# Optimization experiments

Measured on AMD Instinct MI355X. Metric: run time of the kernel, lower is better.

The kernel has to match this reference:

```python
import jax, jax.numpy as jnp
import numpy as np

B, N, NFEAT, NHID, NOUT, H = 16, 1024, 128, 256, 256, 4
DH = NOUT // H  # 64 per head
EPS = 1e-5
ALPHA = 0.2  # LeakyReLU negative slope


def setup_inputs() -> dict:
    key = jax.random.key(0)
    ks = jax.random.split(key, 8)
    stdv = 1.0 / np.sqrt(NHID)
    return {
        "x": jax.random.normal(ks[0], (B, N, NFEAT), dtype=jnp.float32),
        "adj": jax.random.uniform(ks[1], (N, N), dtype=jnp.float32) / N,
        "gc_w": jax.random.uniform(ks[2], (NFEAT, NHID), minval=-stdv, maxval=stdv, dtype=jnp.float32),
        "gc_b": jax.random.uniform(ks[3], (NHID,), minval=-stdv, maxval=stdv, dtype=jnp.float32),
        "bn1_gamma": jnp.ones((NHID,), jnp.float32),
        "bn1_beta": jnp.zeros((NHID,), jnp.float32),
        "gat_w": jax.random.normal(ks[4], (H, NHID, DH), dtype=jnp.float32) * (1.0 / np.sqrt(NHID)),
        "conv_w": jax.random.normal(ks[5], (NOUT, NOUT, 3), dtype=jnp.float32) * (1.0 / np.sqrt(NOUT * 3)),
        "conv_b": jnp.zeros((NOUT,), jnp.float32),
        "bn2_gamma": jnp.ones((NOUT,), jnp.float32),
        "bn2_beta": jnp.zeros((NOUT,), jnp.float32),
    }


def reference(x, adj, gc_w, gc_b, bn1_gamma, bn1_beta, gat_w, conv_w, conv_b, bn2_gamma, bn2_beta):
    # --- GraphConvolution: adj @ (x @ W) + b, relu ---
    h = jnp.einsum("bnf,fo->bno", x, gc_w)
    h = jnp.einsum("nm,bmo->bno", adj, h) + gc_b
    h = jax.nn.relu(h)
    # --- BatchNorm1d over channel dim (training-mode batch stats), relu ---
    mu = h.mean((0, 1))
    var = h.var((0, 1))
    h = (h - mu) * jax.lax.rsqrt(var + EPS) * bn1_gamma + bn1_beta
    h = jax.nn.relu(h)
    # --- Multi-head GAT: per head hp, e = hp hp^T, leakyrelu, softmax, attn @ hp ---
    hp = jnp.einsum("bnf,hfd->bhnd", h, gat_w)          # (B,H,N,DH)
    e = jnp.einsum("bhnd,bhmd->bhnm", hp, hp)            # (B,H,N,N)
    e = jnp.where(e > 0, e, ALPHA * e)
    attn = jax.nn.softmax(e, axis=-1)
    out = jnp.einsum("bhnm,bhmd->bhnd", attn, hp)        # = sum_m attn * hp (the B,N,N,d repeat in torch)
    out = out.transpose(0, 2, 1, 3).reshape(B, N, H * DH)  # concat heads -> (B,N,NOUT)
    # --- TCN block: conv1d (k=3, pad 1) over node axis, batchnorm, relu (dropout=eval) ---
    xc = out.transpose(0, 2, 1)                          # (B,C,N)
    y = jax.lax.conv_general_dilated(xc, conv_w, (1,), [(1, 1)],
                                     dimension_numbers=("NCH", "OIH", "NCH"))
    y = y + conv_b[None, :, None]
    mu2 = y.mean((0, 2), keepdims=True)
    var2 = y.var((0, 2), keepdims=True)
    y = (y - mu2) * jax.lax.rsqrt(var2 + EPS) * bn2_gamma[None, :, None] + bn2_beta[None, :, None]
    y = jax.nn.relu(y)
    return y.transpose(0, 2, 1)                          # (B,N,NOUT)
```

## Files before the change

kernel.cpp:

```cpp
#include <hip/hip_runtime.h>
#include <hip/hip_bf16.h>


typedef unsigned short u16;
typedef __attribute__((ext_vector_type(8))) short short8;
typedef __attribute__((ext_vector_type(4))) float f32x4;

static __device__ __forceinline__ float4 ld4(const float* p){ return *(const float4*)p; }
static __device__ __forceinline__ void st4(float* p, float4 v){ *(float4*)p = v; }

static __device__ __forceinline__ u16 f2bf(float f){
  unsigned u = __builtin_bit_cast(unsigned, f);
  unsigned r = u + 0x7FFFu + ((u >> 16) & 1u);
  return (u16)(r >> 16);
}
static __device__ __forceinline__ float bf2f(u16 h){
  unsigned u = ((unsigned)h) << 16; return __builtin_bit_cast(float, u);
}
static __device__ __forceinline__ void st4bf(u16* p, u16 a, u16 b, u16 c, u16 d){
  uint2 v; v.x = (unsigned)a | ((unsigned)b << 16); v.y = (unsigned)c | ((unsigned)d << 16);
  *(uint2*)p = v;
}
static __device__ __forceinline__ f32x4 mfma16(short8 a, short8 b, f32x4 c){
  return __builtin_amdgcn_mfma_f32_16x16x32_bf16(a, b, c, 0, 0, 0);
}

template<int SPLIT, int K, int NN, int MODE, int AXSWAP, int BM, int BN, int WR, int WC>
static __device__ __forceinline__ void mgemm_body(
    const u16* __restrict__ Ah_, const u16* __restrict__ Al_,
    const u16* __restrict__ Bh_, const u16* __restrict__ Bl_,
    const u16* __restrict__ zbuf,
    void* __restrict__ C0v, void* __restrict__ C1v, void* __restrict__ C2v,
    const float* __restrict__ bias)
{
  constexpr int KT = K / 32;
  constexpr int WM = BM / WR, WN = BN / WC;
  constexpr int MI = WM / 16, NJ = WN / 16;
  __shared__ u16 Ah[BM * 32], Bh[BN * 32];
  __shared__ u16 Al[SPLIT == 3 ? BM * 32 : 8], Bl[SPLIT == 3 ? BN * 32 : 8];
  const int tid = threadIdx.x;
  const int n0 = (AXSWAP ? blockIdx.y : blockIdx.x) * BN;
  const int m0 = (AXSWAP ? blockIdx.x : blockIdx.y) * BM;
  const int lane = tid & 63, l15 = lane & 15, lq = lane >> 4;
  const int w = tid >> 6, wr = w / WC, wc = w % WC;

  f32x4 acc[MI][NJ] = {};

  for (int kt = 0; kt < KT; ++kt){
    const int k0 = kt * 32;
#pragma unroll
    for (int r = 0; r < BM / 64; ++r){
      const int slot = r * 256 + tid;
      const int row = slot & (BM - 1), kh = slot / BM;
      const int ldsoff = (r * 256 + (tid & 192)) * 8;
      const u16* asrc;
      if constexpr (MODE == 3){
        const int kz = k0 >> 8;
        const int ci0 = (k0 & 255) + kh * 8;
        const int R = m0 + row;
        const int nn = (R & 1023) + kz - 1;
        asrc = ((unsigned)nn < 1024u) ? (Ah_ + (size_t)(R + kz - 1) * 256 + ci0) : zbuf;
      } else {
        asrc = Ah_ + (size_t)(m0 + row) * K + k0 + kh * 8;
      }
      __builtin_amdgcn_global_load_lds(asrc, &Ah[ldsoff], 16, 0, 0);
      if constexpr (SPLIT == 3){
        const u16* asrc2 = Al_ + (size_t)(m0 + row) * K + k0 + kh * 8;
        __builtin_amdgcn_global_load_lds(asrc2, &Al[ldsoff], 16, 0, 0);
      }
    }
#pragma unroll
    for (int r = 0; r < BN / 64; ++r){
      const int slot = r * 256 + tid;
      const int row = slot & (BN - 1), kh = slot / BN;
      const int ldsoff = (r * 256 + (tid & 192)) * 8;
      const u16* bsrc = Bh_ + (size_t)(n0 + row) * K + k0 + kh * 8;
      __builtin_amdgcn_global_load_lds(bsrc, &Bh[ldsoff], 16, 0, 0);
      if constexpr (SPLIT == 3){
        const u16* bsrc2 = Bl_ + (size_t)(n0 + row) * K + k0 + kh * 8;
        __builtin_amdgcn_global_load_lds(bsrc2, &Bl[ldsoff], 16, 0, 0);
      }
    }
    __syncthreads();
    short8 afh[MI], bfh[NJ], afl[MI], bfl[NJ];
#pragma unroll
    for (int f = 0; f < MI; ++f){
      afh[f] = *(const short8*)&Ah[(lq * BM + wr * WM + f * 16 + l15) * 8];
      if constexpr (SPLIT == 3)
        afl[f] = *(const short8*)&Al[(lq * BM + wr * WM + f * 16 + l15) * 8];
    }
#pragma unroll
    for (int f = 0; f < NJ; ++f){
      bfh[f] = *(const short8*)&Bh[(lq * BN + wc * WN + f * 16 + l15) * 8];
      if constexpr (SPLIT == 3)
        bfl[f] = *(const short8*)&Bl[(lq * BN + wc * WN + f * 16 + l15) * 8];
    }
#pragma unroll
    for (int fi = 0; fi < MI; ++fi)
#pragma unroll
      for (int fj = 0; fj < NJ; ++fj){
        acc[fi][fj] = mfma16(afh[fi], bfh[fj], acc[fi][fj]);
        if constexpr (SPLIT == 3){
          acc[fi][fj] = mfma16(afl[fi], bfh[fj], acc[fi][fj]);
          acc[fi][fj] = mfma16(afh[fi], bfl[fj], acc[fi][fj]);
        }
      }
    __syncthreads();
  }

  const int rb = m0 + wr * WM;
  const int cb = n0 + wc * WN;
  if constexpr (MODE == 0){
    u16* H = (u16*)C0v; u16* L = (u16*)C1v;
#pragma unroll
    for (int fi = 0; fi < MI; ++fi){
      const int R = rb + fi * 16 + lq * 4;
      const int nn = R & 1023, bq = R >> 10;
#pragma unroll
      for (int fj = 0; fj < NJ; ++fj){
        const int c = cb + fj * 16 + l15;
        const size_t off = (size_t)(bq * 256 + c) * 1024 + nn;
        u16 h_[4], l_[4];
#pragma unroll
        for (int r = 0; r < 4; ++r){
          float v = acc[fi][fj][r];
          u16 hi = f2bf(v); h_[r] = hi; l_[r] = f2bf(v - bf2f(hi));
        }
        st4bf(H + off, h_[0], h_[1], h_[2], h_[3]);
        st4bf(L + off, l_[0], l_[1], l_[2], l_[3]);
      }
    }
  } else if constexpr (MODE == 1){
    float* G = (float*)C0v;
#pragma unroll
    for (int fj = 0; fj < NJ; ++fj){
      const int c = cb + fj * 16 + l15;
      const int o = c & 255, bq = c >> 8;
      const float bs = bias[o];
#pragma unroll
      for (int fi = 0; fi < MI; ++fi){
        const int R = rb + fi * 16 + lq * 4;
#pragma unroll
        for (int r = 0; r < 4; ++r)
          G[((size_t)bq * 1024 + R + r) * 256 + o] = fmaxf(acc[fi][fj][r] + bs, 0.f);
      }
    }
  } else if constexpr (MODE == 2){
    u16* H = (u16*)C0v; u16* L = (u16*)C1v; u16* T = (u16*)C2v;
#pragma unroll
    for (int fi = 0; fi < MI; ++fi){
      const int R = rb + fi * 16 + lq * 4;
#pragma unroll
      for (int fj = 0; fj < NJ; ++fj){
        const int c = cb + fj * 16 + l15;
        u16 h_[4];
#pragma unroll
        for (int r = 0; r < 4; ++r){
          float v = acc[fi][fj][r];
          u16 hi = f2bf(v); h_[r] = hi;
          H[(size_t)(R + r) * 256 + c] = hi;
          L[(size_t)(R + r) * 256 + c] = f2bf(v - bf2f(hi));
        }
        st4bf(T + (size_t)c * 16384 + R, h_[0], h_[1], h_[2], h_[3]);
      }
    }
  } else {
    float* Y = (float*)C0v;
#pragma unroll
    for (int fj = 0; fj < NJ; ++fj){
      const int c = cb + fj * 16 + l15;
      const float bs = bias[c];
#pragma unroll
      for (int fi = 0; fi < MI; ++fi){
        const int R = rb + fi * 16 + lq * 4;
#pragma unroll
        for (int r = 0; r < 4; ++r)
          Y[(size_t)(R + r) * 256 + c] = acc[fi][fj][r] + bs;
      }
    }
  }
}

__global__ __launch_bounds__(256) void gemm0_k(
    const u16* __restrict__ Ah_, const u16* __restrict__ Bh_,
    const u16* __restrict__ zbuf, void* __restrict__ C0, void* __restrict__ C1)
{ mgemm_body<1, 128, 256, 0, 0, 128, 64, 2, 2>(Ah_, nullptr, Bh_, nullptr, zbuf, C0, C1, nullptr, nullptr); }

__global__ __launch_bounds__(256) void gemm1_k(
    const u16* __restrict__ Ah_, const u16* __restrict__ Al_,
    const u16* __restrict__ Bh_, const u16* __restrict__ Bl_,
    const u16* __restrict__ zbuf, void* __restrict__ C0, const float* __restrict__ bias)
{ mgemm_body<3, 1024, 4096, 1, 1, 64, 128, 1, 4>(Ah_, Al_, Bh_, Bl_, zbuf, C0, nullptr, nullptr, bias); }

__global__ __launch_bounds__(256) void gemm2_k(
    const u16* __restrict__ Ah_, const u16* __restrict__ Al_,
    const u16* __restrict__ Bh_, const u16* __restrict__ Bl_,
    const u16* __restrict__ zbuf,
    void* __restrict__ C0, void* __restrict__ C1, void* __restrict__ C2)
{ mgemm_body<3, 256, 256, 2, 0, 128, 64, 2, 2>(Ah_, Al_, Bh_, Bl_, zbuf, C0, C1, C2, nullptr); }

__global__ __launch_bounds__(256) void gemm3_k(
    const u16* __restrict__ Ah_, const u16* __restrict__ Bh_,
    const u16* __restrict__ zbuf, void* __restrict__ C0, const float* __restrict__ bias)
{ mgemm_body<1, 768, 256, 3, 0, 128, 64, 2, 2>(Ah_, nullptr, Bh_, nullptr, zbuf, C0, nullptr, nullptr, bias); }

__global__ __launch_bounds__(256) void flash(
    const u16* __restrict__ hp_hi, const u16* __restrict__ hp_lo,
    const u16* __restrict__ hpT, u16* __restrict__ ao)
{
  __shared__ u16 Khi[4096], Klo[4096], Vt[4096];
  __shared__ u16 Pl[4][1024];
  __shared__ float Ls[4][16];
  const int tid = threadIdx.x;
  const int lane = tid & 63, l15 = lane & 15, lq = lane >> 4, w = tid >> 6;
  const int bid = blockIdx.x;
  const int b = bid & 15, k_ = bid >> 4, h = k_ >> 4, qo = k_ & 15;
  const size_t qrow0 = (size_t)b * 1024 + qo * 64 + w * 16;

  short8 qh[2], ql[2];
#pragma unroll
  for (int ks = 0; ks < 2; ++ks){
    const size_t off = (qrow0 + l15) * 256 + h * 64 + ks * 32 + lq * 8;
    qh[ks] = *(const short8*)(hp_hi + off);
    ql[ks] = *(const short8*)(hp_lo + off);
  }

  f32x4 o_[4] = {};
  float ls[4] = {};

  for (int kt = 0; kt < 16; ++kt){
    const int kv0 = kt * 64;
#pragma unroll
    for (int r = 0; r < 2; ++r){
      const int slot = r * 256 + tid;
      const int g1 = slot >> 6, g2 = slot & 63;
      const int ldsoff = (r * 256 + (tid & 192)) * 8;
      const u16* ksrc = hp_hi + ((size_t)b * 1024 + kv0 + g2) * 256 + h * 64 + g1 * 8;
      __builtin_amdgcn_global_load_lds(ksrc, &Khi[ldsoff], 16, 0, 0);
      const u16* ksrc2 = hp_lo + ((size_t)b * 1024 + kv0 + g2) * 256 + h * 64 + g1 * 8;
      __builtin_amdgcn_global_load_lds(ksrc2, &Klo[ldsoff], 16, 0, 0);
      const u16* vsrc = hpT + (size_t)(h * 64 + g2) * 16384 + b * 1024 + kv0 + g1 * 8;
      __builtin_amdgcn_global_load_lds(vsrc, &Vt[ldsoff], 16, 0, 0);
    }
    __syncthreads();

#pragma unroll
    for (int nf = 0; nf < 4; ++nf){
      short8 kf[2], kg[2];
#pragma unroll
      for (int ks = 0; ks < 2; ++ks){
        kf[ks] = *(const short8*)&Khi[((ks * 4 + lq) * 64 + nf * 16 + l15) * 8];
        kg[ks] = *(const short8*)&Klo[((ks * 4 + lq) * 64 + nf * 16 + l15) * 8];
      }
      const int kv = nf * 16 + l15;
      f32x4 s = {};
#pragma unroll
      for (int ks = 0; ks < 2; ++ks){
        s = mfma16(qh[ks], kf[ks], s);
        s = mfma16(ql[ks], kf[ks], s);
        s = mfma16(qh[ks], kg[ks], s);
      }
      const int base = ((kv >> 3) * 16 + lq * 4) * 8 + (kv & 7);
#pragma unroll
      for (int r = 0; r < 4; ++r){
        float v = s[r];
        v = v > 0.f ? v : 0.2f * v;
        const float p = __expf(v - 40.f);
        ls[r] += p;
        Pl[w][base + r * 8] = f2bf(p);
      }
    }

#pragma unroll
    for (int ks = 0; ks < 2; ++ks){
      short8 va[4];
#pragma unroll
      for (int f = 0; f < 4; ++f)
        va[f] = *(const short8*)&Vt[((ks * 4 + lq) * 64 + f * 16 + l15) * 8];
      const short8 pf = *(const short8*)&Pl[w][((ks * 4 + lq) * 16 + l15) * 8];
#pragma unroll
      for (int df = 0; df < 4; ++df)
        o_[df] = mfma16(va[df], pf, o_[df]);
    }
    __syncthreads();
  }

#pragma unroll
  for (int mask = 1; mask < 16; mask <<= 1)
#pragma unroll
    for (int i = 0; i < 4; ++i)
      ls[i] += __shfl_xor(ls[i], mask, 64);
  if (l15 == 0){
#pragma unroll
    for (int r = 0; r < 4; ++r) Ls[w][lq * 4 + r] = ls[r];
  }
  __syncthreads();
  const float inv = 1.0f / Ls[w][l15];

#pragma unroll
  for (int df = 0; df < 4; ++df){
    const size_t addr = (qrow0 + l15) * 256 + h * 64 + df * 16 + lq * 4;
    st4bf(ao + addr,
          f2bf(o_[df][0] * inv), f2bf(o_[df][1] * inv),
          f2bf(o_[df][2] * inv), f2bf(o_[df][3] * inv));
  }
}

__global__ __launch_bounds__(256) void bn_partial(const float* __restrict__ buf,
                                                  float* __restrict__ part)
{
  const int bi = blockIdx.x, t = threadIdx.x;
  const float* p = buf + (size_t)bi * 64 * 256 + t;
  float s = 0.f, q = 0.f;
#pragma unroll 4
  for (int r = 0; r < 64; ++r){ const float v = p[(size_t)r * 256]; s += v; q = fmaf(v, v, q); }
  part[bi * 512 + t] = s;
  part[bi * 512 + 256 + t] = q;
}

__global__ __launch_bounds__(256) void bn_final(const float* __restrict__ part,
                                                const float* __restrict__ gamma,
                                                const float* __restrict__ beta,
                                                float* __restrict__ prm)
{
  const int t = threadIdx.x;
  float s = 0.f, q = 0.f;
#pragma unroll 8
  for (int i = 0; i < 256; ++i){ s += part[i * 512 + t]; q += part[i * 512 + 256 + t]; }
  const float mu = s * (1.f / 16384.f);
  const float var = q * (1.f / 16384.f) - mu * mu;
  prm[t] = mu;
  prm[256 + t] = rsqrtf(var + 1e-5f) * gamma[t];
  prm[512 + t] = beta[t];
}

__global__ __launch_bounds__(256) void bn_apply_split(const float* __restrict__ in,
    u16* __restrict__ H, u16* __restrict__ L, const float* __restrict__ prm)
{
  const int idx = blockIdx.x * 256 + threadIdx.x;
  const size_t off = (size_t)idx * 4;
  const int o = (int)(off & 255);
  const float4 x = ld4(in + off);
  const float4 m = ld4(prm + o), rs = ld4(prm + 256 + o), bt = ld4(prm + 512 + o);
  u16 h_[4], l_[4];
  float v;
  v = fmaxf(fmaf(x.x - m.x, rs.x, bt.x), 0.f); h_[0] = f2bf(v); l_[0] = f2bf(v - bf2f(h_[0]));
  v = fmaxf(fmaf(x.y - m.y, rs.y, bt.y), 0.f); h_[1] = f2bf(v); l_[1] = f2bf(v - bf2f(h_[1]));
  v = fmaxf(fmaf(x.z - m.z, rs.z, bt.z), 0.f); h_[2] = f2bf(v); l_[2] = f2bf(v - bf2f(h_[2]));
  v = fmaxf(fmaf(x.w - m.w, rs.w, bt.w), 0.f); h_[3] = f2bf(v); l_[3] = f2bf(v - bf2f(h_[3]));
  st4bf(H + off, h_[0], h_[1], h_[2], h_[3]);
  st4bf(L + off, l_[0], l_[1], l_[2], l_[3]);
}

__global__ __launch_bounds__(256) void bn_apply(const float* __restrict__ in,
                                                float* __restrict__ outp,
                                                const float* __restrict__ prm)
{
  const int idx = blockIdx.x * 256 + threadIdx.x;
  const size_t off = (size_t)idx * 8;
  const int o = (int)(off & 255);
  const float4 x0 = ld4(in + off),      x1 = ld4(in + off + 4);
  const float4 m0 = ld4(prm + o),       m1 = ld4(prm + o + 4);
  const float4 r0 = ld4(prm + 256 + o), r1 = ld4(prm + 256 + o + 4);
  const float4 b0 = ld4(prm + 512 + o), b1 = ld4(prm + 512 + o + 4);
  float4 y0, y1;
  y0.x = fmaxf(fmaf(x0.x - m0.x, r0.x, b0.x), 0.f);
  y0.y = fmaxf(fmaf(x0.y - m0.y, r0.y, b0.y), 0.f);
  y0.z = fmaxf(fmaf(x0.z - m0.z, r0.z, b0.z), 0.f);
  y0.w = fmaxf(fmaf(x0.w - m0.w, r0.w, b0.w), 0.f);
  y1.x = fmaxf(fmaf(x1.x - m1.x, r1.x, b1.x), 0.f);
  y1.y = fmaxf(fmaf(x1.y - m1.y, r1.y, b1.y), 0.f);
  y1.z = fmaxf(fmaf(x1.z - m1.z, r1.z, b1.z), 0.f);
  y1.w = fmaxf(fmaf(x1.w - m1.w, r1.w, b1.w), 0.f);
  st4(outp + off, y0);
  st4(outp + off + 4, y1);
}

__global__ __launch_bounds__(256) void pack_w(
    const float* __restrict__ x, const float* __restrict__ adj,
    const float* __restrict__ gcw, const float* __restrict__ gatw,
    const float* __restrict__ convw,
    u16* __restrict__ xbf, u16* __restrict__ adjh, u16* __restrict__ adjl,
    u16* __restrict__ w0t, u16* __restrict__ w2th, u16* __restrict__ w2tl,
    u16* __restrict__ cwt, u16* __restrict__ zb)
{
  const int idx = blockIdx.x * 256 + threadIdx.x;
  if (idx < 2097152) xbf[idx] = f2bf(x[idx]);
  if (idx < 1048576){
    const float v = adj[idx];
    const u16 hi = f2bf(v);
    adjh[idx] = hi; adjl[idx] = f2bf(v - bf2f(hi));
  }
  if (idx < 32768){
    const int o = idx >> 7, f = idx & 127;
    w0t[idx] = f2bf(gcw[f * 256 + o]);
  }
  if (idx < 65536){
    const int c = idx >> 8, f = idx & 255;
    const float v = gatw[(c >> 6) * 16384 + f * 64 + (c & 63)];
    const u16 hi = f2bf(v);
    w2th[idx] = hi; w2tl[idx] = f2bf(v - bf2f(hi));
  }
  if (idx < 196608){
    const int co = idx / 768, k = idx - co * 768;
    const int kz = k >> 8, ci = k & 255;
    cwt[idx] = f2bf(convw[co * 768 + ci * 3 + kz]);
  }
  if (idx < 2048) zb[idx] = 0;
}

extern "C" void kernel_launch(void* const* d_in, const int* in_sizes, int n_in,
                              void* d_out, int out_size, void* d_ws, size_t ws_size,
                              hipStream_t stream)
{
  const float* x     = (const float*)d_in[0];
  const float* adj   = (const float*)d_in[1];
  const float* gc_w  = (const float*)d_in[2];
  const float* gc_b  = (const float*)d_in[3];
  const float* bn1g  = (const float*)d_in[4];
  const float* bn1b  = (const float*)d_in[5];
  const float* gatw  = (const float*)d_in[6];
  const float* convw = (const float*)d_in[7];
  const float* convb = (const float*)d_in[8];
  const float* bn2g  = (const float*)d_in[9];
  const float* bn2b  = (const float*)d_in[10];
  char* ws  = (char*)d_ws;
  char* out = (char*)d_out;

  u16* h1t_hi = (u16*)(ws + 0);
  u16* h1t_lo = (u16*)(ws + 8388608);
  u16* x_bf   = (u16*)(ws + 16777216);
  u16* adj_hi = (u16*)(ws + 20971520);
  u16* adj_lo = (u16*)(ws + 23068672);
  u16* hpT    = (u16*)(ws + 16777216);
  u16* w0t    = (u16*)(ws + 25165824);
  u16* w2th   = (u16*)(ws + 25231360);
  u16* w2tl   = (u16*)(ws + 25362432);
  u16* cwt    = (u16*)(ws + 25493504);
  u16* zbuf   = (u16*)(ws + 25886720);
  float* P1   = (float*)(ws + 25890816);
  float* PR1  = (float*)(ws + 26415104);
  float* PR2  = (float*)(ws + 26419200);
  u16* h_hi  = (u16*)(ws + 0);
  u16* h_lo  = (u16*)(ws + 8388608);
  u16* ao    = (u16*)(ws + 0);
  float* g   = (float*)out;
  u16* hp_hi = (u16*)out;
  u16* hp_lo = (u16*)(out + 8388608);
  float* y   = (float*)out;

  pack_w<<<8192, 256, 0, stream>>>(x, adj, gc_w, gatw, convw,
                                   x_bf, adj_hi, adj_lo, w0t, w2th, w2tl, cwt, zbuf);
  gemm0_k<<<dim3(4, 128), 256, 0, stream>>>(x_bf, w0t, zbuf, h1t_hi, h1t_lo);
  gemm1_k<<<dim3(16, 32), 256, 0, stream>>>(adj_hi, adj_lo, h1t_hi, h1t_lo, zbuf, g, gc_b);
  bn_partial<<<256, 256, 0, stream>>>(g, P1);
  bn_final<<<1, 256, 0, stream>>>(P1, bn1g, bn1b, PR1);
  bn_apply_split<<<4096, 256, 0, stream>>>(g, h_hi, h_lo, PR1);
  gemm2_k<<<dim3(4, 128), 256, 0, stream>>>(h_hi, h_lo, w2th, w2tl, zbuf, hp_hi, hp_lo, hpT);
  flash<<<1024, 256, 0, stream>>>(hp_hi, hp_lo, hpT, ao);
  gemm3_k<<<dim3(4, 128), 256, 0, stream>>>(ao, cwt, zbuf, y, convb);
  bn_partial<<<256, 256, 0, stream>>>(y, P1);
  bn_final<<<1, 256, 0, stream>>>(P1, bn2g, bn2b, PR2);
  bn_apply<<<2048, 256, 0, stream>>>(y, y, PR2);
}
```

Before: 314.7 us.

## Fuse BN partial stats into GEMM epilogues and double query rows per flash block

The GEMM1 and GEMM3 epilogues now compute per-column sum and sum-of-squares partials with wave shuffles and write them directly, which removes both bn_partial kernels and their re-read of the activations. GEMM1 also stores its output as a bf16 hi/lo pair instead of fp32, and bn_apply_split reconstructs the values from that pair. The flash kernel now handles 32 query rows per wave (128 per block, 512 blocks), so each K/V tile loaded into LDS serves twice as many queries. The cost is more registers and LDS per block in flash and fewer blocks to fill the GPU.

```diff
diff --git a/kernel.cpp b/kernel.cpp
--- a/kernel.cpp
+++ b/kernel.cpp
@@ -131,18 +131,32 @@
       }
     }
   } else if constexpr (MODE == 1){
-    float* G = (float*)C0v;
+    u16* GH = (u16*)C0v; u16* GL = (u16*)C1v; float* PT = (float*)C2v;
+    const int mb = AXSWAP ? blockIdx.x : blockIdx.y;
 #pragma unroll
     for (int fj = 0; fj < NJ; ++fj){
       const int c = cb + fj * 16 + l15;
       const int o = c & 255, bq = c >> 8;
       const float bs = bias[o];
+      float s = 0.f, q = 0.f;
 #pragma unroll
       for (int fi = 0; fi < MI; ++fi){
         const int R = rb + fi * 16 + lq * 4;
 #pragma unroll
-        for (int r = 0; r < 4; ++r)
-          G[((size_t)bq * 1024 + R + r) * 256 + o] = fmaxf(acc[fi][fj][r] + bs, 0.f);
+        for (int r = 0; r < 4; ++r){
+          const float v = fmaxf(acc[fi][fj][r] + bs, 0.f);
+          s += v; q = fmaf(v, v, q);
+          const u16 hi = f2bf(v);
+          const size_t off = ((size_t)bq * 1024 + R + r) * 256 + o;
+          GH[off] = hi;
+          GL[off] = f2bf(v - bf2f(hi));
+        }
+      }
+      s += __shfl_xor(s, 16, 64); s += __shfl_xor(s, 32, 64);
+      q += __shfl_xor(q, 16, 64); q += __shfl_xor(q, 32, 64);
+      if (lq == 0){
+        PT[mb * 4096 + c]         = s;
+        PT[65536 + mb * 4096 + c] = q;
       }
     }
   } else if constexpr (MODE == 2){
@@ -165,17 +179,28 @@
       }
     }
   } else {
-    float* Y = (float*)C0v;
+    float* Y = (float*)C0v; float* PT = (float*)C2v;
+    const int slot = blockIdx.y * 2 + wr;
 #pragma unroll
     for (int fj = 0; fj < NJ; ++fj){
       const int c = cb + fj * 16 + l15;
       const float bs = bias[c];
+      float s = 0.f, q = 0.f;
 #pragma unroll
       for (int fi = 0; fi < MI; ++fi){
         const int R = rb + fi * 16 + lq * 4;
 #pragma unroll
-        for (int r = 0; r < 4; ++r)
-          Y[(size_t)(R + r) * 256 + c] = acc[fi][fj][r] + bs;
+        for (int r = 0; r < 4; ++r){
+          const float v = acc[fi][fj][r] + bs;
+          s += v; q = fmaf(v, v, q);
+          Y[(size_t)(R + r) * 256 + c] = v;
+        }
+      }
+      s += __shfl_xor(s, 16, 64); s += __shfl_xor(s, 32, 64);
+      q += __shfl_xor(q, 16, 64); q += __shfl_xor(q, 32, 64);
+      if (lq == 0){
+        PT[slot * 256 + c]         = s;
+        PT[65536 + slot * 256 + c] = q;
       }
     }
   }
@@ -189,8 +214,9 @@
 __global__ __launch_bounds__(256) void gemm1_k(
     const u16* __restrict__ Ah_, const u16* __restrict__ Al_,
     const u16* __restrict__ Bh_, const u16* __restrict__ Bl_,
-    const u16* __restrict__ zbuf, void* __restrict__ C0, const float* __restrict__ bias)
-{ mgemm_body<3, 1024, 4096, 1, 1, 64, 128, 1, 4>(Ah_, Al_, Bh_, Bl_, zbuf, C0, nullptr, nullptr, bias); }
+    const u16* __restrict__ zbuf, void* __restrict__ C0, void* __restrict__ C1,
+    void* __restrict__ C2, const float* __restrict__ bias)
+{ mgemm_body<3, 1024, 4096, 1, 1, 64, 128, 1, 4>(Ah_, Al_, Bh_, Bl_, zbuf, C0, C1, C2, bias); }
 
 __global__ __launch_bounds__(256) void gemm2_k(
     const u16* __restrict__ Ah_, const u16* __restrict__ Al_,
@@ -201,32 +227,35 @@
 
 __global__ __launch_bounds__(256) void gemm3_k(
     const u16* __restrict__ Ah_, const u16* __restrict__ Bh_,
-    const u16* __restrict__ zbuf, void* __restrict__ C0, const float* __restrict__ bias)
-{ mgemm_body<1, 768, 256, 3, 0, 128, 64, 2, 2>(Ah_, nullptr, Bh_, nullptr, zbuf, C0, nullptr, nullptr, bias); }
+    const u16* __restrict__ zbuf, void* __restrict__ C0, void* __restrict__ C2,
+    const float* __restrict__ bias)
+{ mgemm_body<1, 768, 256, 3, 0, 128, 64, 2, 2>(Ah_, nullptr, Bh_, nullptr, zbuf, C0, nullptr, C2, bias); }
 
 __global__ __launch_bounds__(256) void flash(
     const u16* __restrict__ hp_hi, const u16* __restrict__ hp_lo,
     const u16* __restrict__ hpT, u16* __restrict__ ao)
 {
   __shared__ u16 Khi[4096], Klo[4096], Vt[4096];
-  __shared__ u16 Pl[4][1024];
-  __shared__ float Ls[4][16];
+  __shared__ u16 Pl[4][2048];
+  __shared__ float Ls[4][32];
   const int tid = threadIdx.x;
   const int lane = tid & 63, l15 = lane & 15, lq = lane >> 4, w = tid >> 6;
   const int bid = blockIdx.x;
-  const int b = bid & 15, k_ = bid >> 4, h = k_ >> 4, qo = k_ & 15;
-  const size_t qrow0 = (size_t)b * 1024 + qo * 64 + w * 16;
-
-  short8 qh[2], ql[2];
-#pragma unroll
-  for (int ks = 0; ks < 2; ++ks){
-    const size_t off = (qrow0 + l15) * 256 + h * 64 + ks * 32 + lq * 8;
-    qh[ks] = *(const short8*)(hp_hi + off);
-    ql[ks] = *(const short8*)(hp_lo + off);
-  }
-
-  f32x4 o_[4] = {};
-  float ls[4] = {};
+  const int b = bid & 15, k_ = bid >> 4, h = k_ >> 3, qo = k_ & 7;
+  const size_t qrow0 = (size_t)b * 1024 + qo * 128 + w * 32;
+
+  short8 qh[2][2], ql[2][2];
+#pragma unroll
+  for (int mf = 0; mf < 2; ++mf)
+#pragma unroll
+    for (int ks = 0; ks < 2; ++ks){
+      const size_t off = (qrow0 + mf * 16 + l15) * 256 + h * 64 + ks * 32 + lq * 8;
+      qh[mf][ks] = *(const short8*)(hp_hi + off);
+      ql[mf][ks] = *(const short8*)(hp_lo + off);
+    }
+
+  f32x4 o_[4][2] = {};
+  float ls[8] = {};
 
   for (int kt = 0; kt < 16; ++kt){
     const int kv0 = kt * 64;
@@ -253,34 +282,42 @@
         kg[ks] = *(const short8*)&Klo[((ks * 4 + lq) * 64 + nf * 16 + l15) * 8];
       }
       const int kv = nf * 16 + l15;
-      f32x4 s = {};
-#pragma unroll
-      for (int ks = 0; ks < 2; ++ks){
-        s = mfma16(qh[ks], kf[ks], s);
-        s = mfma16(ql[ks], kf[ks], s);
-        s = mfma16(qh[ks], kg[ks], s);
-      }
-      const int base = ((kv >> 3) * 16 + lq * 4) * 8 + (kv & 7);
-#pragma unroll
-      for (int r = 0; r < 4; ++r){
-        float v = s[r];
-        v = v > 0.f ? v : 0.2f * v;
-        const float p = __expf(v - 40.f);
-        ls[r] += p;
-        Pl[w][base + r * 8] = f2bf(p);
+#pragma unroll
+      for (int mf = 0; mf < 2; ++mf){
+        f32x4 s = {};
+#pragma unroll
+        for (int ks = 0; ks < 2; ++ks){
+          s = mfma16(qh[mf][ks], kf[ks], s);
+          s = mfma16(ql[mf][ks], kf[ks], s);
+          s = mfma16(qh[mf][ks], kg[ks], s);
+        }
+        const int qb = mf * 16 + lq * 4;
+        const int base = ((kv >> 3) * 32 + qb) * 8 + (kv & 7);
+#pragma unroll
+        for (int r = 0; r < 4; ++r){
+          float v = s[r];
+          v = v > 0.f ? v : 0.2f * v;
+          const float p = __expf(v - 40.f);
+          ls[mf * 4 + r] += p;
+          Pl[w][base + r * 8] = f2bf(p);
+        }
       }
     }
 
 #pragma unroll
     for (int ks = 0; ks < 2; ++ks){
-      short8 va[4];
+      short8 va[4], pf[2];
 #pragma unroll
       for (int f = 0; f < 4; ++f)
         va[f] = *(const short8*)&Vt[((ks * 4 + lq) * 64 + f * 16 + l15) * 8];
-      const short8 pf = *(const short8*)&Pl[w][((ks * 4 + lq) * 16 + l15) * 8];
+#pragma unroll
+      for (int f = 0; f < 2; ++f)
+        pf[f] = *(const short8*)&Pl[w][((ks * 4 + lq) * 32 + f * 16 + l15) * 8];
 #pragma unroll
       for (int df = 0; df < 4; ++df)
-        o_[df] = mfma16(va[df], pf, o_[df]);
+#pragma unroll
+        for (int qf = 0; qf < 2; ++qf)
+          o_[df][qf] = mfma16(va[df], pf[qf], o_[df][qf]);
     }
     __syncthreads();
   }
@@ -288,34 +325,29 @@
 #pragma unroll
   for (int mask = 1; mask < 16; mask <<= 1)
 #pragma unroll
-    for (int i = 0; i < 4; ++i)
+    for (int i = 0; i < 8; ++i)
       ls[i] += __shfl_xor(ls[i], mask, 64);
   if (l15 == 0){
 #pragma unroll
-    for (int r = 0; r < 4; ++r) Ls[w][lq * 4 + r] = ls[r];
+    for (int mf = 0; mf < 2; ++mf)
+#pragma unroll
+      for (int r = 0; r < 4; ++r)
+        Ls[w][mf * 16 + lq * 4 + r] = ls[mf * 4 + r];
   }
   __syncthreads();
-  const float inv = 1.0f / Ls[w][l15];
-
-#pragma unroll
-  for (int df = 0; df < 4; ++df){
-    const size_t addr = (qrow0 + l15) * 256 + h * 64 + df * 16 + lq * 4;
-    st4bf(ao + addr,
-          f2bf(o_[df][0] * inv), f2bf(o_[df][1] * inv),
-          f2bf(o_[df][2] * inv), f2bf(o_[df][3] * inv));
-  }
-}
-
-__global__ __launch_bounds__(256) void bn_partial(const float* __restrict__ buf,
-                                                  float* __restrict__ part)
-{
-  const int bi = blockIdx.x, t = threadIdx.x;
-  const float* p = buf + (size_t)bi * 64 * 256 + t;
-  float s = 0.f, q = 0.f;
-#pragma unroll 4
-  for (int r = 0; r < 64; ++r){ const float v = p[(size_t)r * 256]; s += v; q = fmaf(v, v, q); }
-  part[bi * 512 + t] = s;
-  part[bi * 512 + 256 + t] = q;
+  float inv[2];
+#pragma unroll
+  for (int qf = 0; qf < 2; ++qf) inv[qf] = 1.0f / Ls[w][qf * 16 + l15];
+
+#pragma unroll
+  for (int qf = 0; qf < 2; ++qf)
+#pragma unroll
+    for (int df = 0; df < 4; ++df){
+      const size_t addr = (qrow0 + qf * 16 + l15) * 256 + h * 64 + df * 16 + lq * 4;
+      st4bf(ao + addr,
+            f2bf(o_[df][qf][0] * inv[qf]), f2bf(o_[df][qf][1] * inv[qf]),
+            f2bf(o_[df][qf][2] * inv[qf]), f2bf(o_[df][qf][3] * inv[qf]));
+    }
 }
 
 __global__ __launch_bounds__(256) void bn_final(const float* __restrict__ part,
@@ -326,7 +358,7 @@
   const int t = threadIdx.x;
   float s = 0.f, q = 0.f;
 #pragma unroll 8
-  for (int i = 0; i < 256; ++i){ s += part[i * 512 + t]; q += part[i * 512 + 256 + t]; }
+  for (int i = 0; i < 256; ++i){ s += part[i * 256 + t]; q += part[65536 + i * 256 + t]; }
   const float mu = s * (1.f / 16384.f);
   const float var = q * (1.f / 16384.f) - mu * mu;
   prm[t] = mu;
@@ -334,20 +366,26 @@
   prm[512 + t] = beta[t];
 }
 
-__global__ __launch_bounds__(256) void bn_apply_split(const float* __restrict__ in,
+__global__ __launch_bounds__(256) void bn_apply_split(
+    const u16* __restrict__ GH, const u16* __restrict__ GL,
     u16* __restrict__ H, u16* __restrict__ L, const float* __restrict__ prm)
 {
   const int idx = blockIdx.x * 256 + threadIdx.x;
   const size_t off = (size_t)idx * 4;
   const int o = (int)(off & 255);
-  const float4 x = ld4(in + off);
+  const uint2 hv = *(const uint2*)(GH + off);
+  const uint2 lv = *(const uint2*)(GL + off);
   const float4 m = ld4(prm + o), rs = ld4(prm + 256 + o), bt = ld4(prm + 512 + o);
+  float x0 = bf2f((u16)(hv.x & 0xffff)) + bf2f((u16)(lv.x & 0xffff));
+  float x1 = bf2f((u16)(hv.x >> 16))    + bf2f((u16)(lv.x >> 16));
+  float x2 = bf2f((u16)(hv.y & 0xffff)) + bf2f((u16)(lv.y & 0xffff));
+  float x3 = bf2f((u16)(hv.y >> 16))    + bf2f((u16)(lv.y >> 16));
   u16 h_[4], l_[4];
   float v;
-  v = fmaxf(fmaf(x.x - m.x, rs.x, bt.x), 0.f); h_[0] = f2bf(v); l_[0] = f2bf(v - bf2f(h_[0]));
-  v = fmaxf(fmaf(x.y - m.y, rs.y, bt.y), 0.f); h_[1] = f2bf(v); l_[1] = f2bf(v - bf2f(h_[1]));
-  v = fmaxf(fmaf(x.z - m.z, rs.z, bt.z), 0.f); h_[2] = f2bf(v); l_[2] = f2bf(v - bf2f(h_[2]));
-  v = fmaxf(fmaf(x.w - m.w, rs.w, bt.w), 0.f); h_[3] = f2bf(v); l_[3] = f2bf(v - bf2f(h_[3]));
+  v = fmaxf(fmaf(x0 - m.x, rs.x, bt.x), 0.f); h_[0] = f2bf(v); l_[0] = f2bf(v - bf2f(h_[0]));
+  v = fmaxf(fmaf(x1 - m.y, rs.y, bt.y), 0.f); h_[1] = f2bf(v); l_[1] = f2bf(v - bf2f(h_[1]));
+  v = fmaxf(fmaf(x2 - m.z, rs.z, bt.z), 0.f); h_[2] = f2bf(v); l_[2] = f2bf(v - bf2f(h_[2]));
+  v = fmaxf(fmaf(x3 - m.w, rs.w, bt.w), 0.f); h_[3] = f2bf(v); l_[3] = f2bf(v - bf2f(h_[3]));
   st4bf(H + off, h_[0], h_[1], h_[2], h_[3]);
   st4bf(L + off, l_[0], l_[1], l_[2], l_[3]);
 }
@@ -444,7 +482,8 @@
   u16* h_hi  = (u16*)(ws + 0);
   u16* h_lo  = (u16*)(ws + 8388608);
   u16* ao    = (u16*)(ws + 0);
-  float* g   = (float*)out;
+  u16* g_hi  = (u16*)out;
+  u16* g_lo  = (u16*)(out + 8388608);
   u16* hp_hi = (u16*)out;
   u16* hp_lo = (u16*)(out + 8388608);
   float* y   = (float*)out;
@@ -452,14 +491,13 @@
   pack_w<<<8192, 256, 0, stream>>>(x, adj, gc_w, gatw, convw,
                                    x_bf, adj_hi, adj_lo, w0t, w2th, w2tl, cwt, zbuf);
   gemm0_k<<<dim3(4, 128), 256, 0, stream>>>(x_bf, w0t, zbuf, h1t_hi, h1t_lo);
-  gemm1_k<<<dim3(16, 32), 256, 0, stream>>>(adj_hi, adj_lo, h1t_hi, h1t_lo, zbuf, g, gc_b);
-  bn_partial<<<256, 256, 0, stream>>>(g, P1);
+  gemm1_k<<<dim3(16, 32), 256, 0, stream>>>(adj_hi, adj_lo, h1t_hi, h1t_lo, zbuf,
+                                            g_hi, g_lo, P1, gc_b);
   bn_final<<<1, 256, 0, stream>>>(P1, bn1g, bn1b, PR1);
-  bn_apply_split<<<4096, 256, 0, stream>>>(g, h_hi, h_lo, PR1);
+  bn_apply_split<<<4096, 256, 0, stream>>>(g_hi, g_lo, h_hi, h_lo, PR1);
   gemm2_k<<<dim3(4, 128), 256, 0, stream>>>(h_hi, h_lo, w2th, w2tl, zbuf, hp_hi, hp_lo, hpT);
-  flash<<<1024, 256, 0, stream>>>(hp_hi, hp_lo, hpT, ao);
-  gemm3_k<<<dim3(4, 128), 256, 0, stream>>>(ao, cwt, zbuf, y, convb);
-  bn_partial<<<256, 256, 0, stream>>>(y, P1);
+  flash<<<512, 256, 0, stream>>>(hp_hi, hp_lo, hpT, ao);
+  gemm3_k<<<dim3(4, 128), 256, 0, stream>>>(ao, cwt, zbuf, y, P1, convb);
   bn_final<<<1, 256, 0, stream>>>(P1, bn2g, bn2b, PR2);
   bn_apply<<<2048, 256, 0, stream>>>(y, y, PR2);
 }
```

Result: faster. 301.5 us (-4.2%).
